# Performance work log

Measured on AMD Instinct MI355X. Metric: run time of the kernel, lower is better.

## Reference

```python
import jax, jax.numpy as jnp
import numpy as np
from jax import lax

P = 8          # patch_size
K = 2          # active_experts
EPS = 1e-5     # LayerNorm eps


def _expert(xp, dw_w, dw_b, ln_g, ln_b, pwin_w, pwin_b, pwout_w, pwout_b):
    # xp: [N, C, L, P, P]  -- one GatedConvBlock (use_cbam=False, no cond)
    N, C, L, Ph, Pw = xp.shape
    res = xp
    # depthwise (1,7,7) conv == 2D depthwise 7x7 per time step: fold L into batch
    x2 = xp.transpose(0, 2, 1, 3, 4).reshape(N * L, C, Ph, Pw)
    y = lax.conv_general_dilated(
        x2, dw_w, window_strides=(1, 1), padding=[(3, 3), (3, 3)],
        feature_group_count=C, dimension_numbers=('NCHW', 'OIHW', 'NCHW'))
    y = y + dw_b[None, :, None, None]
    # LayerNorm over spatial (P,P) per (n, l, c); affine params are [P,P]
    mu = y.mean(axis=(-2, -1), keepdims=True)
    var = ((y - mu) ** 2).mean(axis=(-2, -1), keepdims=True)
    y = (y - mu) * lax.rsqrt(var + EPS) * ln_g + ln_b
    # pointwise in: C -> 2C, SiLU gate, pointwise out: C -> C
    h = jnp.einsum('nchw,dc->ndhw', y, pwin_w) + pwin_b[None, :, None, None]
    a, g = jnp.split(h, 2, axis=1)
    h = jax.nn.silu(a) * g
    o = jnp.einsum('nchw,dc->ndhw', h, pwout_w) + pwout_b[None, :, None, None]
    return res + o.reshape(N, L, C, Ph, Pw).transpose(0, 2, 1, 3, 4)


def setup_inputs() -> dict:
    key = jax.random.key(0)
    ks = jax.random.split(key, 8)
    B, C, L, H, W = 2, 64, 8, 160, 160
    E = 8
    x = jax.random.normal(ks[0], (B, C, L, H, W), dtype=jnp.float32)
    router_w = jax.random.normal(ks[1], (E, C), dtype=jnp.float32) * 0.05
    router_b = jnp.zeros((E,), dtype=jnp.float32)
    dw_w = jax.random.normal(ks[2], (E, C, 1, 7, 7), dtype=jnp.float32) * 0.05
    dw_b = jnp.zeros((E, C), dtype=jnp.float32)
    ln_g = jnp.ones((E, P, P), dtype=jnp.float32)
    ln_b = jnp.zeros((E, P, P), dtype=jnp.float32)
    pwin_w = jax.random.normal(ks[3], (E, 2 * C, C), dtype=jnp.float32) * 0.05
    pwin_b = jnp.zeros((E, 2 * C), dtype=jnp.float32)
    pwout_w = jax.random.normal(ks[4], (E, C, C), dtype=jnp.float32) * 0.05
    pwout_b = jnp.zeros((E, C), dtype=jnp.float32)
    return {"x": x, "router_w": router_w, "router_b": router_b,
            "dw_w": dw_w, "dw_b": dw_b, "ln_g": ln_g, "ln_b": ln_b,
            "pwin_w": pwin_w, "pwin_b": pwin_b,
            "pwout_w": pwout_w, "pwout_b": pwout_b}


def reference(x, router_w, router_b, dw_w, dw_b, ln_g, ln_b,
              pwin_w, pwin_b, pwout_w, pwout_b):
    B, C, L, H, W = x.shape
    E = router_b.shape[0]
    # H, W divisible by P here -> no padding branch
    nH, nW = H // P, W // P
    # extract patches: [B*nH*nW, C, L, P, P]
    xp = (x.reshape(B, C, L, nH, P, nW, P)
           .transpose(0, 3, 5, 1, 2, 4, 6)
           .reshape(-1, C, L, P, P))
    N = xp.shape[0]
    # router over pooled patch features
    router_in = xp.mean(axis=(2, 3, 4))                       # [N, C]
    logits = router_in @ router_w.T + router_b                # [N, E]
    topk_logits, topk_idx = lax.top_k(logits, K)              # [N, K]
    topk_w = jax.nn.softmax(topk_logits, axis=1)              # [N, K]
    # combine weights: [N, E], zero where expert not selected
    combine = (jax.nn.one_hot(topk_idx, E, dtype=x.dtype) * topk_w[..., None]).sum(axis=1)
    # dispatch/combine via scan over experts (weighted sum == torch masked index_add)
    def body(acc, p):
        dw_w_e, dw_b_e, g_e, b_e, pi_w, pi_b, po_w, po_b, w_e = p
        y = _expert(xp, dw_w_e, dw_b_e, g_e, b_e, pi_w, pi_b, po_w, po_b)
        return acc + w_e[:, None, None, None, None] * y, None
    out, _ = lax.scan(body, jnp.zeros_like(xp),
                      (dw_w, dw_b, ln_g, ln_b, pwin_w, pwin_b,
                       pwout_w, pwout_b, combine.T))
    # reassemble patches -> [B, C, L, H, W]
    output = (out.reshape(B, nH, nW, C, L, P, P)
                 .transpose(0, 3, 4, 1, 5, 2, 6)
                 .reshape(B, C, L, H, W))
    return output
```

## Files before the change

kernel.cpp:

```cpp
#include <hip/hip_runtime.h>

#define NB 2
#define CCH 64
#define LL 8
#define HH 160
#define WW 160
#define PP 8
#define NPH 20
#define NPW 20
#define NPAT 800
#define NE 8
#define HWX 25600
#define CSTRIDE 204800

typedef float f32x4  __attribute__((ext_vector_type(4)));
typedef float f32x16 __attribute__((ext_vector_type(16)));
typedef short bf16x8 __attribute__((ext_vector_type(8)));

__device__ __host__ __forceinline__ unsigned short f2bf(float f) {
    unsigned u = __builtin_bit_cast(unsigned, f);
    u = (u + 0x7FFFu + ((u >> 16) & 1u)) >> 16;
    return (unsigned short)u;
}
__device__ __forceinline__ unsigned cvtpk(float lo, float hi) {
    unsigned r;
    asm("v_cvt_pk_bf16_f32 %0, %1, %2" : "=v"(r) : "v"(lo), "v"(hi));
    return r;
}
__device__ __forceinline__ float dpp_xor1(float v) {
    int s = __builtin_bit_cast(int, v);
    return __builtin_bit_cast(float, __builtin_amdgcn_update_dpp(s, s, 0xB1, 0xF, 0xF, false));
}
__device__ __forceinline__ int xsw(int s) { return ((s & 7) ^ ((s >> 3) & 7)) << 2; }

__global__ __launch_bounds__(256)
void prep_kernel(const float* __restrict__ pwin_w, const float* __restrict__ pwout_w,
                 const float* __restrict__ dw_w,
                 unsigned short* __restrict__ w1t, unsigned short* __restrict__ w2t,
                 unsigned short* __restrict__ tbl)
{
    int idx = blockIdx.x * 256 + threadIdx.x;
    {
        int j = idx & 7, lane = (idx >> 3) & 63, ks2 = (idx >> 9) & 3;
        int po = (idx >> 11) & 31, e = (idx >> 16) & 7;
        int m16 = lane & 15;
        int ch = m16 >> 3, jout = m16 & 7;
        int k128 = ks2*32 + ((lane >> 4) << 3) + j;
        int kc = k128 >> 6, k64 = k128 & 63;
        int di = k64 >> 3, jj = k64 & 7;
        int dj = jj - jout + 3;
        int h = po >> 4, mm = po & 15;
        int c = 32*h + mm + ch*16;
        float v = 0.f;
        if (kc == ch && di < 7 && dj >= 0 && dj < 7)
            v = dw_w[(e*CCH + c)*49 + di*7 + dj];
        tbl[idx] = f2bf(v);
    }
    if (idx < NE*128*64) {
        int e = idx >> 13, r = (idx >> 6) & 127, c = idx & 63;
        int orig = (r & 1) ? 64 + (r >> 1) : (r >> 1);
        w1t[idx] = f2bf(pwin_w[(e << 13) + orig*64 + c]);
    }
    if (idx < NE*64*64) w2t[idx] = f2bf(pwout_w[idx]);
}

__global__ __launch_bounds__(256)
void router_sum(const float* __restrict__ x, float* __restrict__ pmean2)
{
    int bid = blockIdx.x;
    int ph = bid % 20;
    int r  = bid / 20;
    int l  = r % 8;
    int b  = r / 8;

    __shared__ float acc[1280];
    const float* base = x + ((size_t)(b*CCH)*LL + l)*HWX + (size_t)(ph*PP)*WW;
    int t = threadIdx.x;

    #pragma unroll
    for (int k = 0; k < 5; ++k) {
        int s = t + 256*k;
        int pw = s % 20, c = s / 20;
        const float* rp = base + (size_t)c*CSTRIDE + pw*8;
        float sum = 0.f;
        #pragma unroll
        for (int i = 0; i < 8; ++i) {
            float4 v0 = *(const float4*)(rp + i*WW);
            float4 v1 = *(const float4*)(rp + i*WW + 4);
            sum += v0.x+v0.y+v0.z+v0.w + v1.x+v1.y+v1.z+v1.w;
        }
        acc[c*20 + pw] = sum;
    }
    __syncthreads();
    #pragma unroll
    for (int k = 0; k < 5; ++k) {
        int s = t + 256*k;
        int c = s & 63, pwi = s >> 6;
        int n = b*400 + ph*20 + pwi;
        pmean2[(size_t)n*512 + l*64 + c] = acc[c*20 + pwi];
    }
}

__global__ __launch_bounds__(64)
void router_top(const float* __restrict__ pmean2,
                const float* __restrict__ rw, const float* __restrict__ rb,
                int* __restrict__ sel_idx, float* __restrict__ sel_w)
{
    int n = blockIdx.x;
    int t = threadIdx.x;
    __shared__ float mc[64];
    __shared__ float lg[8];
    const float* pb = pmean2 + (size_t)n*512;
    float s = 0.f;
    #pragma unroll
    for (int l = 0; l < 8; ++l) s += pb[l*64 + t];
    mc[t] = s * (1.f/512.f);
    __syncthreads();
    if (t < 8) {
        float a = rb[t];
        for (int c = 0; c < 64; ++c) a += mc[c] * rw[t*64 + c];
        lg[t] = a;
    }
    __syncthreads();
    if (t == 0) {
        float m0 = -1e30f; int i0 = 0;
        #pragma unroll
        for (int e = 0; e < NE; ++e) { float v = lg[e]; if (v > m0) { m0 = v; i0 = e; } }
        float m1 = -1e30f; int i1 = 0;
        #pragma unroll
        for (int e = 0; e < NE; ++e) { if (e != i0) { float v = lg[e]; if (v > m1) { m1 = v; i1 = e; } } }
        float dd = __expf(m1 - m0);
        float inv = 1.f / (1.f + dd);
        sel_idx[n*2]   = i0;  sel_idx[n*2+1] = i1;
        sel_w[n*2]     = inv; sel_w[n*2+1]   = dd * inv;
    }
}

__global__ __launch_bounds__(256, 2)
void moe_v12(const float* __restrict__ x,
             const float* __restrict__ ln_g,
             const float* __restrict__ ln_b,
             const float* __restrict__ pwin_b,
             const float* __restrict__ pwout_b,
             const unsigned short* __restrict__ w1t,
             const unsigned short* __restrict__ w2t,
             const unsigned short* __restrict__ tbl,
             const int* __restrict__ sel_idx,
             const float* __restrict__ sel_w,
             float* __restrict__ out)
{
    __shared__ __align__(16) unsigned smem[16400];
    unsigned* xs = smem;
    float* obuf  = (float*)smem;

    int bid = blockIdx.x;
    int xg = bid & 7, pp = (bid >> 3) & 1, w = bid >> 4;
    int b = xg >> 2, lp = xg & 3;
    int ph = w / 5, pwh = w - ph*5;
    int pwq = pwh*2 + pp;

    int t = threadIdx.x;
    int lane = t & 63;
    int wv = __builtin_amdgcn_readfirstlane(t >> 6);
    int p = wv & 1;
    int h = wv >> 1;
    int col16 = lane & 15, grp = lane >> 4;
    int io = col16 & 7, l2n = col16 >> 3;
    int laneM = lane & 31, hi = lane >> 5;
    bool oddl = (lane & 1) != 0;
    int srow_b = (oddl ? 32 : 0) + 4*hi;
    int sx = (h & 1) << 2;

    size_t xpb = ((size_t)(b*CCH)*LL + lp*2)*HWX + (size_t)(ph*PP)*WW + pwq*16;
    int np = b*400 + ph*20 + pwq*2 + p;

    if (t < 16) smem[16384 + t] = 0u;

    #pragma unroll
    for (int k = 0; k < 16; ++k) {
        int id = t + 256*k;
        int part = id & 3, i = (id >> 2) & 7, l2s = (id >> 5) & 1, c = id >> 6;
        const float* rp = x + xpb + (size_t)c*CSTRIDE + (size_t)l2s*HWX + i*WW + part*4;
        float4 v = *(const float4*)rp;
        uint2 bu;
        bu.x = cvtpk(v.x, v.y);
        bu.y = cvtpk(v.z, v.w);
        int off = (part*2) ^ (((l2s ^ (i >> 2)) & 1) << 2);
        *(uint2*)&xs[c*128 + l2s*64 + i*8 + off] = bu;
    }
    __syncthreads();

    int e0 = __builtin_amdgcn_readfirstlane(sel_idx[np*2]);
    int e1 = __builtin_amdgcn_readfirstlane(sel_idx[np*2+1]);
    float wA = sel_w[np*2], wB = sel_w[np*2+1];

    f32x16 oacc[2][2];
    #pragma unroll
    for (int st = 0; st < 2; ++st)
        #pragma unroll
        for (int ct = 0; ct < 2; ++ct)
            #pragma unroll
            for (int i = 0; i < 16; ++i) oacc[st][ct][i] = 0.f;

    unsigned* sl = smem + 8192 + (p*2 + h)*2048;

    int rowoff[2]; bool okr[2];
    #pragma unroll
    for (int ks = 0; ks < 2; ++ks) {
        int row = io + ks*4 + grp - 3;
        int rw = row & 7;
        rowoff[ks] = l2n*64 + rw*8 + (((p ^ l2n ^ (rw >> 2)) & 1) << 2);
        okr[ks] = (unsigned)row < 8u;
    }
    int sb = io*8 + (grp & 1)*4;
    int chs = grp >> 1;
    int sp2 = p*2 + l2n;
    int csx = l2n << 2;

    #pragma unroll 1
    for (int pass = 0; pass < 2; ++pass) {
        int e    = pass ? e1 : e0;
        float we = pass ? wB : wA;

        const unsigned short* te = tbl + (((size_t)(e*32 + h*16)) << 11);
        float gv[4], bv[4];
        #pragma unroll
        for (int r = 0; r < 4; ++r) {
            gv[r] = ln_g[e*64 + sb + r];
            bv[r] = ln_b[e*64 + sb + r];
        }

        #pragma unroll 2
        for (int m = 0; m < 16; ++m) {
            int cA = 32*h + m;
            const unsigned short* tm = te + ((size_t)m << 11);
            f32x4 ac; ac[0]=0.f; ac[1]=0.f; ac[2]=0.f; ac[3]=0.f;
            #pragma unroll
            for (int ks2 = 0; ks2 < 4; ++ks2) {
                int c = cA + ((ks2 & 2) ? 16 : 0);
                int ks = ks2 & 1;
                int aB = okr[ks] ? (c*128 + rowoff[ks]) : 16384;
                uint4 bu = *(const uint4*)&xs[aB];
                uint4 af = *(const uint4*)(tm + ks2*512 + lane*8);
                ac = __builtin_amdgcn_mfma_f32_16x16x32_bf16(
                    __builtin_bit_cast(bf16x8, af), __builtin_bit_cast(bf16x8, bu), ac, 0, 0, 0);
            }
            float sum = ac[0]+ac[1]+ac[2]+ac[3];
            float sq  = 0.f;
            #pragma unroll
            for (int r = 0; r < 4; ++r) sq = fmaf(ac[r], ac[r], sq);
            sum += __shfl_xor(sum, 1);  sq += __shfl_xor(sq, 1);
            sum += __shfl_xor(sum, 2);  sq += __shfl_xor(sq, 2);
            sum += __shfl_xor(sum, 4);  sq += __shfl_xor(sq, 4);
            sum += __shfl_xor(sum, 16); sq += __shfl_xor(sq, 16);
            float mu  = sum * 0.015625f;
            float var = fmaxf(fmaf(sq, 0.015625f, -mu*mu), 0.f);
            float inv = rsqrtf(var + 1e-5f);
            float nmu = -mu * inv;
            int myc = cA + (chs ? 16 : 0);
            unsigned short* Yh = (unsigned short*)smem;
            int cd = (myc >> 1), cb = myc & 1;
            #pragma unroll
            for (int r = 0; r < 4; ++r) {
                float y = fmaf(fmaf(ac[r], inv, nmu), gv[r], bv[r]);
                int s = sb + r;
                int dw = 8192 + sp2*2048 + s*32 + ((cd ^ xsw(s)) ^ csx);
                Yh[dw*2 + cb] = (unsigned short)cvtpk(y, y);
            }
        }
        __syncthreads();

        uint4 aY0[4], aY1[4];
        #pragma unroll
        for (int ks = 0; ks < 4; ++ks) {
            int kd = 8*ks + 4*hi;
            aY0[ks] = *(const uint4*)&sl[laneM*32 + ((kd ^ xsw(laneM)) ^ sx)];
            aY1[ks] = *(const uint4*)&sl[(32 + laneM)*32 + ((kd ^ xsw(32 + laneM)) ^ sx)];
        }
        const unsigned short* w1e = w1t + ((size_t)e << 13);
        const unsigned short* w2e = w2t + ((size_t)e << 12);

        #pragma unroll 1
        for (int dt = 0; dt < 4; ++dt) {
            uint4 b1f[4];
            #pragma unroll
            for (int ks = 0; ks < 4; ++ks)
                b1f[ks] = *(const uint4*)(w1e + (32*dt + laneM)*64 + 16*ks + 8*hi);
            int dp = 32*dt + laneM;
            int borig = (dp & 1) ? 64 + (dp >> 1) : (dp >> 1);
            float bias1 = pwin_b[e*128 + borig];

            f32x16 acc0, acc1;
            #pragma unroll
            for (int i = 0; i < 16; ++i) { acc0[i]=0.f; acc1[i]=0.f; }
            #pragma unroll
            for (int ks = 0; ks < 4; ++ks) {
                bf16x8 bvf = __builtin_bit_cast(bf16x8, b1f[ks]);
                acc0 = __builtin_amdgcn_mfma_f32_32x32x16_bf16(
                    __builtin_bit_cast(bf16x8, aY0[ks]), bvf, acc0, 0, 0, 0);
                acc1 = __builtin_amdgcn_mfma_f32_32x32x16_bf16(
                    __builtin_bit_cast(bf16x8, aY1[ks]), bvf, acc1, 0, 0, 0);
            }
            int kg  = 16*dt + (laneM >> 1);
            int kdg = kg >> 1, kbit = kg & 1;
            #pragma unroll
            for (int r = 0; r < 16; ++r) {
                float h0 = acc0[r] + bias1;
                float h1 = acc1[r] + bias1;
                float p0 = dpp_xor1(h0);
                float p1 = dpp_xor1(h1);
                float A = oddl ? p1 : h0;
                float G = oddl ? h1 : p0;
                float sg = __builtin_amdgcn_rcpf(1.f + __expf(-A));
                float val = A * sg * G;
                int srow = srow_b + (r & 3) + 8*(r >> 2);
                int dwg = srow*32 + ((kdg ^ xsw(srow)) ^ sx);
                ((unsigned short*)sl)[dwg*2 + kbit] = (unsigned short)cvtpk(val, val);
            }
        }
        #pragma unroll
        for (int ct = 0; ct < 2; ++ct) {
            int cn = 32*ct + laneM;
            uint4 b2f[4];
            #pragma unroll
            for (int ks = 0; ks < 4; ++ks)
                b2f[ks] = *(const uint4*)(w2e + cn*64 + 16*ks + 8*hi);
            float bias2 = pwout_b[e*64 + cn];
            #pragma unroll
            for (int st = 0; st < 2; ++st) {
                f32x16 g;
                #pragma unroll
                for (int i = 0; i < 16; ++i) g[i] = 0.f;
                #pragma unroll
                for (int ks = 0; ks < 4; ++ks) {
                    int sG = 32*st + laneM;
                    int kd = 8*ks + 4*hi;
                    uint4 ag = *(const uint4*)&sl[sG*32 + ((kd ^ xsw(sG)) ^ sx)];
                    g = __builtin_amdgcn_mfma_f32_32x32x16_bf16(
                        __builtin_bit_cast(bf16x8, ag), __builtin_bit_cast(bf16x8, b2f[ks]), g, 0, 0, 0);
                }
                #pragma unroll
                for (int i = 0; i < 16; ++i)
                    oacc[st][ct][i] = fmaf(we, g[i] + bias2, oacc[st][ct][i]);
            }
        }
        __syncthreads();
    }

    {
        float* obr = obuf + (p*2 + h)*4096;
        #pragma unroll
        for (int st = 0; st < 2; ++st)
            #pragma unroll
            for (int ct = 0; ct < 2; ++ct)
                #pragma unroll
                for (int r = 0; r < 16; ++r) {
                    int c = 32*ct + laneM;
                    int s = 32*st + 4*hi + (r & 3) + 8*(r >> 2);
                    obr[c*64 + (s ^ c)] = oacc[st][ct][r];
                }
        __syncthreads();
        #pragma unroll
        for (int rr = 0; rr < 16; ++rr) {
            int row = rr*64 + (t >> 2);
            int l2s = row >> 9;
            int rem = row & 511;
            int c = rem >> 3, i = rem & 7;
            int q4 = (t & 3) * 4;
            int pq = q4 >> 3;
            int jb = q4 & 7;
            int ob = (pq*2 + l2s)*4096 + c*64;
            float4 v;
            v.x = obuf[ob + ((i*8 + jb + 0) ^ c)];
            v.y = obuf[ob + ((i*8 + jb + 1) ^ c)];
            v.z = obuf[ob + ((i*8 + jb + 2) ^ c)];
            v.w = obuf[ob + ((i*8 + jb + 3) ^ c)];
            size_t ga = xpb + (size_t)c*CSTRIDE + (size_t)l2s*HWX + i*WW + q4;
            float4 xr = *(const float4*)(x + ga);
            v.x += xr.x; v.y += xr.y; v.z += xr.z; v.w += xr.w;
            *(float4*)(out + ga) = v;
        }
    }
}

extern "C" void kernel_launch(void* const* d_in, const int* in_sizes, int n_in,
                              void* d_out, int out_size, void* d_ws, size_t ws_size,
                              hipStream_t stream) {
    const float* x        = (const float*)d_in[0];
    const float* router_w = (const float*)d_in[1];
    const float* router_b = (const float*)d_in[2];
    const float* dw_w     = (const float*)d_in[3];
    const float* ln_g     = (const float*)d_in[5];
    const float* ln_b     = (const float*)d_in[6];
    const float* pwin_w   = (const float*)d_in[7];
    const float* pwin_b   = (const float*)d_in[8];
    const float* pwout_w  = (const float*)d_in[9];
    const float* pwout_b  = (const float*)d_in[10];
    float* out = (float*)d_out;

    char* ws = (char*)d_ws;
    int*            sel_idx = (int*)ws;
    float*          sel_w   = (float*)(ws + 6400);
    unsigned short* w1t     = (unsigned short*)(ws + 12800);
    unsigned short* w2t     = (unsigned short*)(ws + 143872);
    unsigned short* tbl     = (unsigned short*)(ws + 209408);
    float*          pmean2  = (float*)(ws + 1257984);

    prep_kernel<<<2048, 256, 0, stream>>>(pwin_w, pwout_w, dw_w, w1t, w2t, tbl);
    router_sum<<<320, 256, 0, stream>>>(x, pmean2);
    router_top<<<NPAT, 64, 0, stream>>>(pmean2, router_w, router_b, sel_idx, sel_w);
    moe_v12<<<1600, 256, 0, stream>>>(x, ln_g, ln_b, pwin_b, pwout_b,
                                      w1t, w2t, tbl, sel_idx, sel_w, out);
}
```

Baseline: 176.3 us.

## Pre-convert x to tiled bf16 in router pass and read it directly in new MoE kernel

The router reduction pass now also writes a bf16 copy of x in a per-patch-tile layout. A new moe_v13 kernel reads depthwise-conv B operands straight from that global buffer, using a zero page for out-of-range rows, instead of staging x through shared memory. This shrinks shared memory so the kernel can run 3 blocks per CU. The trade-off is an extra ~52MB write plus a re-read, and the path only runs if the workspace is large enough, otherwise it falls back to v12.

```diff
diff --git a/kernel.cpp b/kernel.cpp
--- a/kernel.cpp
+++ b/kernel.cpp
@@ -37,7 +37,7 @@
 void prep_kernel(const float* __restrict__ pwin_w, const float* __restrict__ pwout_w,
                  const float* __restrict__ dw_w,
                  unsigned short* __restrict__ w1t, unsigned short* __restrict__ w2t,
-                 unsigned short* __restrict__ tbl)
+                 unsigned short* __restrict__ tbl, unsigned* __restrict__ zp, int full)
 {
     int idx = blockIdx.x * 256 + threadIdx.x;
     {
@@ -62,16 +62,19 @@
         w1t[idx] = f2bf(pwin_w[(e << 13) + orig*64 + c]);
     }
     if (idx < NE*64*64) w2t[idx] = f2bf(pwout_w[idx]);
+    if (full && idx < 16) zp[idx] = 0u;
 }
 
 __global__ __launch_bounds__(256)
-void router_sum(const float* __restrict__ x, float* __restrict__ pmean2)
+void router_sum(const float* __restrict__ x, float* __restrict__ pmean2,
+                unsigned short* __restrict__ xbf, int do_xbf)
 {
     int bid = blockIdx.x;
     int ph = bid % 20;
     int r  = bid / 20;
     int l  = r % 8;
     int b  = r / 8;
+    int lp = l >> 1, l2 = l & 1;
 
     __shared__ float acc[1280];
     const float* base = x + ((size_t)(b*CCH)*LL + l)*HWX + (size_t)(ph*PP)*WW;
@@ -82,12 +85,23 @@
         int s = t + 256*k;
         int pw = s % 20, c = s / 20;
         const float* rp = base + (size_t)c*CSTRIDE + pw*8;
+        int pwq = pw >> 1, pp2 = pw & 1;
+        size_t tb = ((((size_t)(b*20 + ph))*10 + pwq)*4 + lp)*16384
+                    + (size_t)c*256 + l2*128 + pp2*8;
         float sum = 0.f;
         #pragma unroll
         for (int i = 0; i < 8; ++i) {
             float4 v0 = *(const float4*)(rp + i*WW);
             float4 v1 = *(const float4*)(rp + i*WW + 4);
             sum += v0.x+v0.y+v0.z+v0.w + v1.x+v1.y+v1.z+v1.w;
+            if (do_xbf) {
+                uint4 wv;
+                wv.x = cvtpk(v0.x, v0.y);
+                wv.y = cvtpk(v0.z, v0.w);
+                wv.z = cvtpk(v1.x, v1.y);
+                wv.w = cvtpk(v1.z, v1.w);
+                *(uint4*)(xbf + tb + i*16) = wv;
+            }
         }
         acc[c*20 + pw] = sum;
     }
@@ -133,6 +147,241 @@
         float inv = 1.f / (1.f + dd);
         sel_idx[n*2]   = i0;  sel_idx[n*2+1] = i1;
         sel_w[n*2]     = inv; sel_w[n*2+1]   = dd * inv;
+    }
+}
+
+__global__ __launch_bounds__(256, 3)
+void moe_v13(const float* __restrict__ x,
+             const float* __restrict__ ln_g,
+             const float* __restrict__ ln_b,
+             const float* __restrict__ pwin_b,
+             const float* __restrict__ pwout_b,
+             const unsigned short* __restrict__ w1t,
+             const unsigned short* __restrict__ w2t,
+             const unsigned short* __restrict__ tbl,
+             const unsigned short* __restrict__ xbf,
+             const unsigned short* __restrict__ zp,
+             const int* __restrict__ sel_idx,
+             const float* __restrict__ sel_w,
+             float* __restrict__ out)
+{
+    __shared__ __align__(16) unsigned smem[8224];
+    float* obuf = (float*)smem;
+
+    int bid = blockIdx.x;
+    int xg = bid & 7, pp = (bid >> 3) & 1, w = bid >> 4;
+    int b = xg >> 2, lp = xg & 3;
+    int ph = w / 5, pwh = w - ph*5;
+    int pwq = pwh*2 + pp;
+
+    int t = threadIdx.x;
+    int lane = t & 63;
+    int wv = __builtin_amdgcn_readfirstlane(t >> 6);
+    int p = wv & 1;
+    int h = wv >> 1;
+    int col16 = lane & 15, grp = lane >> 4;
+    int io = col16 & 7, l2n = col16 >> 3;
+    int laneM = lane & 31, hi = lane >> 5;
+    bool oddl = (lane & 1) != 0;
+    int srow_b = (oddl ? 32 : 0) + 4*hi;
+    int sx = (h & 1) << 2;
+
+    size_t xpb = ((size_t)(b*CCH)*LL + lp*2)*HWX + (size_t)(ph*PP)*WW + pwq*16;
+    int np = b*400 + ph*20 + pwq*2 + p;
+    int Tidx = ((b*20 + ph)*10 + pwq)*4 + lp;
+    const unsigned short* xt = xbf + (size_t)Tidx*16384;
+
+    int e0 = __builtin_amdgcn_readfirstlane(sel_idx[np*2]);
+    int e1 = __builtin_amdgcn_readfirstlane(sel_idx[np*2+1]);
+    float wA = sel_w[np*2], wB = sel_w[np*2+1];
+
+    f32x16 oacc[2][2];
+    #pragma unroll
+    for (int st = 0; st < 2; ++st)
+        #pragma unroll
+        for (int ct = 0; ct < 2; ++ct)
+            #pragma unroll
+            for (int i = 0; i < 16; ++i) oacc[st][ct][i] = 0.f;
+
+    unsigned* sl = smem + (p*2 + h)*2056;
+
+    int loff[2]; bool okr[2];
+    #pragma unroll
+    for (int ks = 0; ks < 2; ++ks) {
+        int row = io + ks*4 + grp - 3;
+        loff[ks] = l2n*128 + (row & 7)*16 + p*8;
+        okr[ks] = (unsigned)row < 8u;
+    }
+    int sb = io*8 + (grp & 1)*4;
+    int chs = grp >> 1;
+    int sp2 = p*2 + l2n;
+    int csx = l2n << 2;
+
+    #pragma unroll 1
+    for (int pass = 0; pass < 2; ++pass) {
+        int e    = pass ? e1 : e0;
+        float we = pass ? wB : wA;
+
+        const unsigned short* te = tbl + (((size_t)(e*32 + h*16)) << 11);
+        float gv[4], bv[4];
+        #pragma unroll
+        for (int r = 0; r < 4; ++r) {
+            gv[r] = ln_g[e*64 + sb + r];
+            bv[r] = ln_b[e*64 + sb + r];
+        }
+
+        #pragma unroll 2
+        for (int m = 0; m < 16; ++m) {
+            int cA = 32*h + m;
+            const unsigned short* tm = te + ((size_t)m << 11);
+            f32x4 ac; ac[0]=0.f; ac[1]=0.f; ac[2]=0.f; ac[3]=0.f;
+            #pragma unroll
+            for (int ks2 = 0; ks2 < 4; ++ks2) {
+                int cc = cA + ((ks2 & 2) ? 16 : 0);
+                int ks = ks2 & 1;
+                const unsigned short* bp = okr[ks] ? (xt + cc*256 + loff[ks]) : zp;
+                uint4 bu = *(const uint4*)bp;
+                uint4 af = *(const uint4*)(tm + ks2*512 + lane*8);
+                ac = __builtin_amdgcn_mfma_f32_16x16x32_bf16(
+                    __builtin_bit_cast(bf16x8, af), __builtin_bit_cast(bf16x8, bu), ac, 0, 0, 0);
+            }
+            float sum = ac[0]+ac[1]+ac[2]+ac[3];
+            float sq  = 0.f;
+            #pragma unroll
+            for (int r = 0; r < 4; ++r) sq = fmaf(ac[r], ac[r], sq);
+            sum += __shfl_xor(sum, 1);  sq += __shfl_xor(sq, 1);
+            sum += __shfl_xor(sum, 2);  sq += __shfl_xor(sq, 2);
+            sum += __shfl_xor(sum, 4);  sq += __shfl_xor(sq, 4);
+            sum += __shfl_xor(sum, 16); sq += __shfl_xor(sq, 16);
+            float mu  = sum * 0.015625f;
+            float var = fmaxf(fmaf(sq, 0.015625f, -mu*mu), 0.f);
+            float inv = rsqrtf(var + 1e-5f);
+            float nmu = -mu * inv;
+            int myc = cA + (chs ? 16 : 0);
+            unsigned short* Yh = (unsigned short*)smem;
+            int cd = (myc >> 1), cb = myc & 1;
+            #pragma unroll
+            for (int r = 0; r < 4; ++r) {
+                float y = fmaf(fmaf(ac[r], inv, nmu), gv[r], bv[r]);
+                int s = sb + r;
+                int dw = sp2*2056 + s*32 + ((cd ^ xsw(s)) ^ csx);
+                Yh[dw*2 + cb] = (unsigned short)cvtpk(y, y);
+            }
+        }
+        __syncthreads();
+
+        uint4 aY0[4], aY1[4];
+        #pragma unroll
+        for (int ks = 0; ks < 4; ++ks) {
+            int kd = 8*ks + 4*hi;
+            aY0[ks] = *(const uint4*)&sl[laneM*32 + ((kd ^ xsw(laneM)) ^ sx)];
+            aY1[ks] = *(const uint4*)&sl[(32 + laneM)*32 + ((kd ^ xsw(32 + laneM)) ^ sx)];
+        }
+        const unsigned short* w1e = w1t + ((size_t)e << 13);
+        const unsigned short* w2e = w2t + ((size_t)e << 12);
+
+        #pragma unroll 1
+        for (int dt = 0; dt < 4; ++dt) {
+            uint4 b1f[4];
+            #pragma unroll
+            for (int ks = 0; ks < 4; ++ks)
+                b1f[ks] = *(const uint4*)(w1e + (32*dt + laneM)*64 + 16*ks + 8*hi);
+            int dp = 32*dt + laneM;
+            int borig = (dp & 1) ? 64 + (dp >> 1) : (dp >> 1);
+            float bias1 = pwin_b[e*128 + borig];
+
+            f32x16 acc0, acc1;
+            #pragma unroll
+            for (int i = 0; i < 16; ++i) { acc0[i]=0.f; acc1[i]=0.f; }
+            #pragma unroll
+            for (int ks = 0; ks < 4; ++ks) {
+                bf16x8 bvf = __builtin_bit_cast(bf16x8, b1f[ks]);
+                acc0 = __builtin_amdgcn_mfma_f32_32x32x16_bf16(
+                    __builtin_bit_cast(bf16x8, aY0[ks]), bvf, acc0, 0, 0, 0);
+                acc1 = __builtin_amdgcn_mfma_f32_32x32x16_bf16(
+                    __builtin_bit_cast(bf16x8, aY1[ks]), bvf, acc1, 0, 0, 0);
+            }
+            int kg  = 16*dt + (laneM >> 1);
+            int kdg = kg >> 1, kbit = kg & 1;
+            #pragma unroll
+            for (int r = 0; r < 16; ++r) {
+                float h0 = acc0[r] + bias1;
+                float h1 = acc1[r] + bias1;
+                float p0 = dpp_xor1(h0);
+                float p1 = dpp_xor1(h1);
+                float A = oddl ? p1 : h0;
+                float G = oddl ? h1 : p0;
+                float sg = __builtin_amdgcn_rcpf(1.f + __expf(-A));
+                float val = A * sg * G;
+                int srow = srow_b + (r & 3) + 8*(r >> 2);
+                int dwg = srow*32 + ((kdg ^ xsw(srow)) ^ sx);
+                ((unsigned short*)sl)[dwg*2 + kbit] = (unsigned short)cvtpk(val, val);
+            }
+        }
+        #pragma unroll
+        for (int ct = 0; ct < 2; ++ct) {
+            int cn = 32*ct + laneM;
+            uint4 b2f[4];
+            #pragma unroll
+            for (int ks = 0; ks < 4; ++ks)
+                b2f[ks] = *(const uint4*)(w2e + cn*64 + 16*ks + 8*hi);
+            float bias2 = pwout_b[e*64 + cn];
+            #pragma unroll
+            for (int st = 0; st < 2; ++st) {
+                f32x16 g;
+                #pragma unroll
+                for (int i = 0; i < 16; ++i) g[i] = 0.f;
+                #pragma unroll
+                for (int ks = 0; ks < 4; ++ks) {
+                    int sG = 32*st + laneM;
+                    int kd = 8*ks + 4*hi;
+                    uint4 ag = *(const uint4*)&sl[sG*32 + ((kd ^ xsw(sG)) ^ sx)];
+                    g = __builtin_amdgcn_mfma_f32_32x32x16_bf16(
+                        __builtin_bit_cast(bf16x8, ag), __builtin_bit_cast(bf16x8, b2f[ks]), g, 0, 0, 0);
+                }
+                #pragma unroll
+                for (int i = 0; i < 16; ++i)
+                    oacc[st][ct][i] = fmaf(we, g[i] + bias2, oacc[st][ct][i]);
+            }
+        }
+        __syncthreads();
+    }
+
+    #pragma unroll 1
+    for (int ph2 = 0; ph2 < 2; ++ph2) {
+        if (h == ph2) {
+            float* obr = obuf + p*4096;
+            #pragma unroll
+            for (int st = 0; st < 2; ++st)
+                #pragma unroll
+                for (int ct = 0; ct < 2; ++ct)
+                    #pragma unroll
+                    for (int r = 0; r < 16; ++r) {
+                        int c = 32*ct + laneM;
+                        int s = 32*st + 4*hi + (r & 3) + 8*(r >> 2);
+                        obr[c*64 + (s ^ c)] = oacc[st][ct][r];
+                    }
+        }
+        __syncthreads();
+        #pragma unroll
+        for (int rr = 0; rr < 8; ++rr) {
+            int row = rr*64 + (t >> 2);
+            int c = row >> 3, i = row & 7;
+            int q4 = (t & 3) * 4;
+            int pq = q4 >> 3;
+            int jb = q4 & 7;
+            int ob = pq*4096 + c*64;
+            float4 v;
+            v.x = obuf[ob + ((i*8 + jb + 0) ^ c)];
+            v.y = obuf[ob + ((i*8 + jb + 1) ^ c)];
+            v.z = obuf[ob + ((i*8 + jb + 2) ^ c)];
+            v.w = obuf[ob + ((i*8 + jb + 3) ^ c)];
+            size_t ga = xpb + (size_t)c*CSTRIDE + (size_t)ph2*HWX + i*WW + q4;
+            float4 xr = *(const float4*)(x + ga);
+            v.x += xr.x; v.y += xr.y; v.z += xr.z; v.w += xr.w;
+            *(float4*)(out + ga) = v;
+        }
+        if (ph2 == 0) __syncthreads();
     }
 }
 
@@ -405,10 +654,21 @@
     unsigned short* w2t     = (unsigned short*)(ws + 143872);
     unsigned short* tbl     = (unsigned short*)(ws + 209408);
     float*          pmean2  = (float*)(ws + 1257984);
-
-    prep_kernel<<<2048, 256, 0, stream>>>(pwin_w, pwout_w, dw_w, w1t, w2t, tbl);
-    router_sum<<<320, 256, 0, stream>>>(x, pmean2);
+    unsigned*       zp      = (unsigned*)(ws + 2896384);
+    unsigned short* xbf     = (unsigned short*)(ws + 2896448);
+
+    const size_t NEED13 = 55325248;
+    int full13 = (ws_size >= NEED13) ? 1 : 0;
+
+    prep_kernel<<<2048, 256, 0, stream>>>(pwin_w, pwout_w, dw_w, w1t, w2t, tbl, zp, full13);
+    router_sum<<<320, 256, 0, stream>>>(x, pmean2, xbf, full13);
     router_top<<<NPAT, 64, 0, stream>>>(pmean2, router_w, router_b, sel_idx, sel_w);
-    moe_v12<<<1600, 256, 0, stream>>>(x, ln_g, ln_b, pwin_b, pwout_b,
-                                      w1t, w2t, tbl, sel_idx, sel_w, out);
-}
+    if (full13) {
+        moe_v13<<<1600, 256, 0, stream>>>(x, ln_g, ln_b, pwin_b, pwout_b,
+                                          w1t, w2t, tbl, xbf, (const unsigned short*)zp,
+                                          sel_idx, sel_w, out);
+    } else {
+        moe_v12<<<1600, 256, 0, stream>>>(x, ln_g, ln_b, pwin_b, pwout_b,
+                                          w1t, w2t, tbl, sel_idx, sel_w, out);
+    }
+}
```

Measured after the change: 376.5 us. 114% more time.
